# Kernel tuning notes

Hardware: AMD Instinct MI355X
Metric: run time of the kernel (lower is better)

## Reference

```python
import jax, jax.numpy as jnp
import numpy as np

C = 1.0          # Poincare ball curvature
EPS = 1e-7       # clamp epsilon used by the torch code


def _expmap0(u, c=C):
    # geoopt PoincareBall.expmap0: tanh(sqrt(c)||u||) * u / (sqrt(c)||u||)
    sc = jnp.sqrt(c)
    n = jnp.maximum(jnp.linalg.norm(u, axis=-1, keepdims=True), 1e-15)
    return jnp.tanh(sc * n) * u / (sc * n)


def _hyp_dist_sq(x, y, c=C):
    # Pairwise squared Poincare distance WITHOUT materializing [nq,nc,d]:
    # d(x,y) = (2/sqrt(c)) * artanh(sqrt(c) * ||mobius_add(-x, y)||)
    # ||mobius_add(-x,y)||^2 expands into dot products and squared norms.
    dot = x @ y.T                                  # [nq, nc]
    xn = jnp.sum(x * x, axis=-1)[:, None]          # [nq, 1]
    yn = jnp.sum(y * y, axis=-1)[None, :]          # [1, nc]
    alpha = 1.0 - 2.0 * c * dot + c * yn
    beta = 1.0 - c * xn
    num_sq = alpha * alpha * xn - 2.0 * alpha * beta * dot + beta * beta * yn
    den = jnp.maximum(1.0 - 2.0 * c * dot + c * c * xn * yn, 1e-15)
    t = jnp.sqrt(c) * jnp.sqrt(jnp.maximum(num_sq, 0.0)) / den
    t = jnp.clip(t, 0.0, 1.0 - EPS)
    d = (2.0 / jnp.sqrt(c)) * jnp.arctanh(t)
    return d * d


def _project(x, We, be, Wh, bh, Ws, bs, scale_h):
    e = x @ We.T + be
    e = e / jnp.linalg.norm(e, axis=-1, keepdims=True)
    h = _expmap0((x @ Wh.T + bh) * scale_h)
    s = x @ Ws.T + bs
    s = s / jnp.linalg.norm(s, axis=-1, keepdims=True)
    return e, h, s


def setup_inputs() -> dict:
    key = jax.random.key(0)
    ks = jax.random.split(key, 12)
    D, NQ, NC = 768, 512, 65536
    def lin(k, out_d, in_d):
        lim = 1.0 / np.sqrt(in_d)
        k1, k2 = jax.random.split(k)
        W = jax.random.uniform(k1, (out_d, in_d), jnp.float32, -lim, lim)
        b = jax.random.uniform(k2, (out_d,), jnp.float32, -lim, lim)
        return W, b
    We, be = lin(ks[0], 32, D)
    Wh, bh = lin(ks[1], 16, D)
    Ws, bs = lin(ks[2], 16, D)
    W1, b1 = lin(ks[3], 32, D)
    W2, b2 = lin(ks[4], 3, 32)
    return {
        'x_q': jax.random.normal(ks[5], (NQ, D), jnp.float32),
        'x_c': jax.random.normal(ks[6], (NC, D), jnp.float32),
        'We': We, 'be': be, 'Wh': Wh, 'bh': bh, 'Ws': Ws, 'bs': bs,
        'scale_h': jnp.float32(0.3),
        'W1': W1, 'b1': b1, 'W2': W2, 'b2': b2,
    }


def reference(x_q, x_c, We, be, Wh, bh, Ws, bs, scale_h, W1, b1, W2, b2):
    # forward() projections for queries and corpus
    q_e, q_h, q_s = _project(x_q, We, be, Wh, bh, Ws, bs, scale_h)
    c_e, c_h, c_s = _project(x_c, We, be, Wh, bh, Ws, bs, scale_h)
    # get_weights(): softplus MLP on raw query embedding -> [nq, 3]
    w = jax.nn.softplus(jax.nn.relu(x_q @ W1.T + b1) @ W2.T + b2)
    # batch_retrieve math, fully vectorized
    dist_e = 2.0 - 2.0 * (q_e @ c_e.T)                       # unit vecs: ||a-b||^2
    dots = jnp.clip(q_s @ c_s.T, -1.0 + EPS, 1.0 - EPS)
    dist_s = jnp.arccos(dots) ** 2
    dist_h = _hyp_dist_sq(q_h, c_h)
    total = w[:, 0:1] * dist_e + w[:, 1:2] * dist_h + w[:, 2:3] * dist_s
    return -total
```

## Files before the change

### kernel.cpp

```cpp
#include <hip/hip_runtime.h>
#include <math.h>

#define NQ 512
#define NC 65536
#define DIM 768
#define PC_ROWS 128

typedef unsigned short u16;
typedef float f32x4 __attribute__((ext_vector_type(4)));
typedef short bf16x8 __attribute__((ext_vector_type(8)));

#define MFMA16(A, B, C) __builtin_amdgcn_mfma_f32_16x16x32_bf16(A, B, C, 0, 0, 0)

__device__ __forceinline__ u16 f2bf(float x) {
  union { float f; unsigned int u; } v; v.f = x;
  unsigned int r = v.u + 0x7fffu + ((v.u >> 16) & 1u);
  return (u16)(r >> 16);
}
__device__ __forceinline__ float bf2f(u16 h) {
  union { unsigned int u; float f; } v; v.u = ((unsigned int)h) << 16;
  return v.f;
}
__device__ __forceinline__ unsigned int pk2(u16 a, u16 b) {
  return (unsigned int)a | ((unsigned int)b << 16);
}

__device__ __forceinline__ float acos_poly(float x) {
  float z = fabsf(x);
  float p = -0.0012624911f;
  p = fmaf(p, z, 0.0066700901f);
  p = fmaf(p, z, -0.0170881256f);
  p = fmaf(p, z, 0.0308918810f);
  p = fmaf(p, z, -0.0501743046f);
  p = fmaf(p, z, 0.0889789874f);
  p = fmaf(p, z, -0.2145988016f);
  p = fmaf(p, z, 1.5707963050f);
  float r = __builtin_amdgcn_sqrtf(1.0f - z) * p;
  return (x < 0.0f) ? (3.14159265358979f - r) : r;
}

__global__ __launch_bounds__(256) void build_wpak(
    const float* __restrict__ We, const float* __restrict__ Ws,
    const float* __restrict__ Wh, u16* __restrict__ wpak)
{
  int id = blockIdx.x * 256 + threadIdx.x;
  int j = id & 7;
  int lane = (id >> 3) & 63;
  int nt = (id >> 9) & 3;
  int kc = id >> 11;
  int o = nt * 16 + (lane & 15);
  int k = kc * 32 + ((lane >> 4) & 3) * 8 + j;
  const float* Wrow = (o < 32) ? We + (size_t)o * DIM
                    : (o < 48) ? Ws + (size_t)(o - 32) * DIM
                               : Wh + (size_t)(o - 48) * DIM;
  float w = Wrow[k];
  u16 hi = f2bf(w);
  u16 lo = f2bf(w - bf2f(hi));
  size_t base = (((size_t)kc * 4 + nt) * 2 * 64 + lane) * 8 + j;
  wpak[base] = hi;
  wpak[base + 512] = lo;
}

__global__ __launch_bounds__(128) void proj_q(
    const float* __restrict__ xq,
    const float* __restrict__ We, const float* __restrict__ be,
    const float* __restrict__ Wh, const float* __restrict__ bh,
    const float* __restrict__ Ws, const float* __restrict__ bs,
    const float* __restrict__ shp,
    const float* __restrict__ W1, const float* __restrict__ b1,
    const float* __restrict__ W2, const float* __restrict__ b2,
    u16* __restrict__ qpak, float* __restrict__ qmeta)
{
  __shared__ __align__(16) float xrow[DIM];
  __shared__ float vals[96];
  __shared__ float reluv[32];
  __shared__ float hv[16];
  __shared__ float stats[8];
  const int t = threadIdx.x;
  const int q = blockIdx.x;

  for (int i = t; i < DIM; i += 128) xrow[i] = xq[(size_t)q * DIM + i];
  __syncthreads();

  if (t < 96) {
    const float* wr;
    float bias;
    if (t < 32)      { wr = We + (size_t)t * DIM;        bias = be[t]; }
    else if (t < 48) { wr = Ws + (size_t)(t - 32) * DIM; bias = bs[t - 32]; }
    else if (t < 64) { wr = Wh + (size_t)(t - 48) * DIM; bias = bh[t - 48]; }
    else             { wr = W1 + (size_t)(t - 64) * DIM; bias = b1[t - 64]; }
    const float4* x4 = (const float4*)xrow;
    const float4* w4 = (const float4*)wr;
    float acc = 0.0f;
    #pragma unroll 4
    for (int k = 0; k < DIM / 4; ++k) {
      float4 a = x4[k];
      float4 b = w4[k];
      acc = fmaf(a.x, b.x, acc);
      acc = fmaf(a.y, b.y, acc);
      acc = fmaf(a.z, b.z, acc);
      acc = fmaf(a.w, b.w, acc);
    }
    acc += bias;
    if (t >= 48 && t < 64) acc *= shp[0];
    vals[t] = acc;
  }
  __syncthreads();
  if (t < 32) reluv[t] = fmaxf(vals[64 + t], 0.0f);
  __syncthreads();

  if (t == 0) {
    float s = 0.0f;
    for (int j = 0; j < 32; ++j) s += vals[j] * vals[j];
    stats[0] = sqrtf(s);
  } else if (t == 1) {
    float s = 0.0f;
    for (int j = 32; j < 48; ++j) s += vals[j] * vals[j];
    stats[1] = sqrtf(s);
  } else if (t == 2) {
    float s = 0.0f;
    for (int j = 48; j < 64; ++j) s += vals[j] * vals[j];
    float n = fmaxf(sqrtf(s), 1e-15f);
    float f = tanhf(n) / n;
    float xn = 0.0f;
    for (int j = 0; j < 16; ++j) {
      float hj = vals[48 + j] * f;
      hv[j] = hj;
      xn += hj * hj;
    }
    stats[2] = xn;
    stats[3] = 1.0f - xn;
  } else if (t >= 3 && t < 6) {
    int m = t - 3;
    float s = 0.0f;
    for (int j = 0; j < 32; ++j) s = fmaf(reluv[j], W2[m * 32 + j], s);
    s += b2[m];
    stats[4 + m] = fmaxf(s, 0.0f) + log1pf(expf(-fabsf(s)));
  }
  __syncthreads();

  u16* qp = qpak + (size_t)q * 192;
  if (t < 32) {
    float v = vals[t] / stats[0];
    u16 hi = f2bf(v);
    u16 lo = f2bf(v - bf2f(hi));
    qp[t] = hi; qp[32 + t] = lo;
  } else if (t < 48) {
    int j = t - 32;
    float v = vals[t] / stats[1];
    u16 hi = f2bf(v);
    u16 lo = f2bf(v - bf2f(hi));
    qp[64 + j] = hi;  qp[80 + j] = hi;
    qp[96 + j] = lo;  qp[112 + j] = lo;
  } else if (t < 64) {
    int j = t - 48;
    float v = hv[j];
    u16 hi = f2bf(v);
    u16 lo = f2bf(v - bf2f(hi));
    qp[128 + j] = hi; qp[144 + j] = hi;
    qp[160 + j] = lo; qp[176 + j] = lo;
  } else if (t == 64) qmeta[(size_t)q * 8 + 0] = stats[2];
  else if (t == 65)   qmeta[(size_t)q * 8 + 1] = stats[3];
  else if (t >= 66 && t < 69) qmeta[(size_t)q * 8 + (t - 66 + 2)] = stats[4 + (t - 66)];
}

__global__ __launch_bounds__(256) void proj_corpus(
    const float* __restrict__ xc, const u16* __restrict__ wpak,
    const float* __restrict__ be, const float* __restrict__ bh,
    const float* __restrict__ bs, const float* __restrict__ shp,
    u16* __restrict__ cpak, float* __restrict__ cyn)
{
  __shared__ float lds[8320];
  u16* xpk = (u16*)lds;
  float (*vals)[65] = (float(*)[65])lds;
  __shared__ float biasc[64];
  __shared__ float shv;

  const int tid = threadIdx.x;
  const int lane = tid & 63;
  const int wv = tid >> 6;
  const int lr = lane & 15;
  const int lg = lane >> 4;
  const int r0 = blockIdx.x * PC_ROWS;

  if (tid < 64) {
    biasc[tid] = (tid < 32) ? be[tid] : (tid < 48) ? bs[tid - 32] : bh[tid - 48];
    if (tid == 0) shv = shp[0];
  }

  f32x4 acc[2][4];
  #pragma unroll
  for (int rt = 0; rt < 2; ++rt)
    #pragma unroll
    for (int nt = 0; nt < 4; ++nt)
      acc[rt][nt] = (f32x4){0.0f, 0.0f, 0.0f, 0.0f};

  for (int kc = 0; kc < 24; ++kc) {
    __syncthreads();
    #pragma unroll
    for (int i = 0; i < 4; ++i) {
      int p = tid + 256 * i;
      int row = p >> 3;
      int kq = p & 7;
      const float4 v = *(const float4*)(xc + (size_t)(r0 + row) * DIM + kc * 32 + 4 * kq);
      u16 hx = f2bf(v.x), hy = f2bf(v.y), hz = f2bf(v.z), hw = f2bf(v.w);
      u16 lx = f2bf(v.x - bf2f(hx)), ly = f2bf(v.y - bf2f(hy));
      u16 lz = f2bf(v.z - bf2f(hz)), lw = f2bf(v.w - bf2f(hw));
      uint2 hvv = {pk2(hx, hy), pk2(hz, hw)};
      uint2 lvv = {pk2(lx, ly), pk2(lz, lw)};
      int rm = row & 7;
      int qh = (kq >> 1) ^ rm;
      int ql = (4 + (kq >> 1)) ^ rm;
      int half = (kq & 1) * 8;
      *(uint2*)((char*)xpk + row * 128 + qh * 16 + half) = hvv;
      *(uint2*)((char*)xpk + row * 128 + ql * 16 + half) = lvv;
    }
    __syncthreads();

    const u16* wb = wpak + (size_t)kc * 4096;
    bf16x8 Bh[4], Bl[4];
    #pragma unroll
    for (int nt = 0; nt < 4; ++nt) {
      Bh[nt] = *(const bf16x8*)(wb + (nt * 2 + 0) * 512 + lane * 8);
      Bl[nt] = *(const bf16x8*)(wb + (nt * 2 + 1) * 512 + lane * 8);
    }

    #pragma unroll
    for (int rt = 0; rt < 2; ++rt) {
      int rowi = wv * 32 + rt * 16 + lr;
      int rm = rowi & 7;
      bf16x8 Ah = *(const bf16x8*)((const char*)xpk + rowi * 128 + (lg ^ rm) * 16);
      bf16x8 Al = *(const bf16x8*)((const char*)xpk + rowi * 128 + ((4 + lg) ^ rm) * 16);
      #pragma unroll
      for (int nt = 0; nt < 4; ++nt) {
        acc[rt][nt] = MFMA16(Ah, Bh[nt], acc[rt][nt]);
        acc[rt][nt] = MFMA16(Al, Bh[nt], acc[rt][nt]);
        acc[rt][nt] = MFMA16(Ah, Bl[nt], acc[rt][nt]);
      }
    }
  }
  __syncthreads();

  #pragma unroll
  for (int rt = 0; rt < 2; ++rt)
    #pragma unroll
    for (int nt = 0; nt < 4; ++nt)
      #pragma unroll
      for (int reg = 0; reg < 4; ++reg) {
        int row = wv * 32 + rt * 16 + lg * 4 + reg;
        int o = nt * 16 + lr;
        float v = acc[rt][nt][reg] + biasc[o];
        if (o >= 48) v *= shv;
        vals[row][o] = v;
      }
  __syncthreads();

  const int part = tid >> 7;
  const int row = tid & 127;
  const size_t g = (size_t)(r0 + row);
  u16* cp = cpak + g * 128;
  if (part == 0) {
    float ssum = 0.0f;
    for (int j = 0; j < 32; ++j) ssum += vals[row][j] * vals[row][j];
    float inv = 1.0f / sqrtf(ssum);
    for (int j = 0; j < 32; ++j) {
      float v = vals[row][j] * inv;
      u16 hi = f2bf(v);
      cp[j] = hi;
      cp[32 + j] = f2bf(v - bf2f(hi));
    }
  } else {
    float ssum = 0.0f;
    for (int j = 32; j < 48; ++j) ssum += vals[row][j] * vals[row][j];
    float inv = 1.0f / sqrtf(ssum);
    for (int j = 0; j < 16; ++j) {
      float v = vals[row][32 + j] * inv;
      u16 hi = f2bf(v);
      cp[64 + j] = hi;
      cp[80 + j] = f2bf(v - bf2f(hi));
    }
    float hsum = 0.0f;
    for (int j = 48; j < 64; ++j) hsum += vals[row][j] * vals[row][j];
    float n = fmaxf(sqrtf(hsum), 1e-15f);
    float f = tanhf(n) / n;
    float yn = 0.0f;
    for (int j = 0; j < 16; ++j) {
      float hj = vals[row][48 + j] * f;
      u16 hi = f2bf(hj);
      cp[96 + j] = hi;
      cp[112 + j] = f2bf(hj - bf2f(hi));
      yn += hj * hj;
    }
    cyn[g] = yn;
  }
}

#define CLIPC 0.99999988f

__device__ __forceinline__ float pair_score(
    float de, float dss, float dh,
    float xn, float beta, float w0, float w1, float w2, float yn)
{
  float dist_e = 2.0f - 2.0f * de;

  float dcl = fminf(fmaxf(dss, -CLIPC), CLIPC);
  float ac = acos_poly(dcl);
  float dist_s = ac * ac;

  float alpha = 1.0f - 2.0f * dh + yn;
  float ab = alpha * beta;
  float num = alpha * alpha * xn - 2.0f * ab * dh + beta * beta * yn;
  float den = fmaxf(1.0f - 2.0f * dh + xn * yn, 1e-15f);
  float t = __builtin_amdgcn_sqrtf(fmaxf(num, 0.0f)) * __builtin_amdgcn_rcpf(den);
  t = fminf(t, CLIPC);
  float dd = __logf((1.0f + t) * __builtin_amdgcn_rcpf(1.0f - t));
  float dist_h = dd * dd;

  return -(w0 * dist_e + w1 * dist_h + w2 * dist_s);
}

__global__ __launch_bounds__(256) void pairwise(
    const u16* __restrict__ cpak, const float* __restrict__ cyn,
    const u16* __restrict__ qpak, const float* __restrict__ qmeta,
    float* __restrict__ out)
{
  const int lane = threadIdx.x & 63;
  const int wv = threadIdx.x >> 6;
  const int lr = lane & 15;
  const int lg = lane >> 4;
  const int c0 = blockIdx.x * 128 + wv * 32;
  const int qbase = blockIdx.y * 256;

  bf16x8 Beh[2], Bel[2], Bsp[2], Bhp[2];
  float ynv[2];
  #pragma unroll
  for (int ct = 0; ct < 2; ++ct) {
    const u16* cb = cpak + (size_t)(c0 + ct * 16 + lr) * 128 + lg * 8;
    Beh[ct] = *(const bf16x8*)(cb + 0);
    Bel[ct] = *(const bf16x8*)(cb + 32);
    Bsp[ct] = *(const bf16x8*)(cb + 64);
    Bhp[ct] = *(const bf16x8*)(cb + 96);
    ynv[ct] = cyn[c0 + ct * 16 + lr];
  }

  #pragma unroll 1
  for (int qt = 0; qt < 16; ++qt) {
    const int q0 = qbase + qt * 16;
    const u16* qb = qpak + (size_t)(q0 + lr) * 192 + lg * 8;
    bf16x8 Aeh = *(const bf16x8*)(qb + 0);
    bf16x8 Ael = *(const bf16x8*)(qb + 32);
    bf16x8 Ash = *(const bf16x8*)(qb + 64);
    bf16x8 Asl = *(const bf16x8*)(qb + 96);
    bf16x8 Ahh = *(const bf16x8*)(qb + 128);
    bf16x8 Ahl = *(const bf16x8*)(qb + 160);

    float4 mv[4];
    float w2v[4];
    #pragma unroll
    for (int j = 0; j < 4; ++j) {
      const int q = q0 + lg * 4 + j;
      mv[j] = *(const float4*)(qmeta + (size_t)q * 8);
      w2v[j] = qmeta[(size_t)q * 8 + 4];
    }

    const f32x4 z = {0.0f, 0.0f, 0.0f, 0.0f};
    f32x4 aE[2], aS[2], aH[2];
    #pragma unroll
    for (int ct = 0; ct < 2; ++ct) {
      aE[ct] = MFMA16(Aeh, Beh[ct], z);
      aE[ct] = MFMA16(Ael, Beh[ct], aE[ct]);
      aE[ct] = MFMA16(Aeh, Bel[ct], aE[ct]);
      aS[ct] = MFMA16(Ash, Bsp[ct], z);
      aS[ct] = MFMA16(Asl, Bsp[ct], aS[ct]);
      aH[ct] = MFMA16(Ahh, Bhp[ct], z);
      aH[ct] = MFMA16(Ahl, Bhp[ct], aH[ct]);
    }

    #pragma unroll
    for (int j = 0; j < 4; ++j) {
      const int q = q0 + lg * 4 + j;
      #pragma unroll
      for (int ct = 0; ct < 2; ++ct) {
        float r = pair_score(aE[ct][j], aS[ct][j], aH[ct][j],
                             mv[j].x, mv[j].y, mv[j].z, mv[j].w, w2v[j],
                             ynv[ct]);
        out[(size_t)q * NC + c0 + ct * 16 + lr] = r;
      }
    }
  }
}

extern "C" void kernel_launch(void* const* d_in, const int* in_sizes, int n_in,
                              void* d_out, int out_size, void* d_ws, size_t ws_size,
                              hipStream_t stream) {
  const float* xq = (const float*)d_in[0];
  const float* xc = (const float*)d_in[1];
  const float* We = (const float*)d_in[2];
  const float* be = (const float*)d_in[3];
  const float* Wh = (const float*)d_in[4];
  const float* bh = (const float*)d_in[5];
  const float* Ws = (const float*)d_in[6];
  const float* bs = (const float*)d_in[7];
  const float* sh = (const float*)d_in[8];
  const float* W1 = (const float*)d_in[9];
  const float* b1 = (const float*)d_in[10];
  const float* W2 = (const float*)d_in[11];
  const float* b2 = (const float*)d_in[12];
  float* out = (float*)d_out;

  float* w = (float*)d_ws;
  u16* qpak = (u16*)w;
  float* qmeta = w + 49152;
  u16* wpak = (u16*)(qmeta + NQ * 8);
  float* base2 = qmeta + NQ * 8 + 49152;
  u16* cpak = (u16*)base2;
  float* cyn = base2 + 4194304;

  build_wpak<<<192, 256, 0, stream>>>(We, Ws, Wh, wpak);
  proj_q<<<NQ, 128, 0, stream>>>(xq, We, be, Wh, bh, Ws, bs, sh, W1, b1, W2, b2,
                                 qpak, qmeta);
  proj_corpus<<<NC / PC_ROWS, 256, 0, stream>>>(xc, wpak, be, bh, bs, sh, cpak, cyn);
  pairwise<<<dim3(NC / 128, 2, 1), 256, 0, stream>>>(cpak, cyn, qpak, qmeta, out);
}
```

Measured before the change: 445.6 us.

## Pipeline corpus projection loads, precompute query metadata, simplify pairwise hyperbolic math

The corpus projection now stages raw fp32 rows into LDS with double-buffered direct global-to-LDS loads, one region per wave, and splits them into bf16 hi/lo pairs at fragment-load time with packed convert instructions. This removes the block-wide barriers and register conversion on the load path. The pairwise kernel caches per-query constants in LDS, prefetches the next query tile's operands, and rewrites the hyperbolic distance algebraically with a precomputed (1+yn) term so fewer ops run per pair. Output stores become nontemporal. The algebraic rewrite and the wider LDS footprint may change rounding and occupancy.

```diff
diff --git a/kernel.cpp b/kernel.cpp
--- a/kernel.cpp
+++ b/kernel.cpp
@@ -7,22 +7,30 @@
 #define PC_ROWS 128
 
 typedef unsigned short u16;
+typedef unsigned int u32;
 typedef float f32x4 __attribute__((ext_vector_type(4)));
 typedef short bf16x8 __attribute__((ext_vector_type(8)));
 
 #define MFMA16(A, B, C) __builtin_amdgcn_mfma_f32_16x16x32_bf16(A, B, C, 0, 0, 0)
 
 __device__ __forceinline__ u16 f2bf(float x) {
-  union { float f; unsigned int u; } v; v.f = x;
-  unsigned int r = v.u + 0x7fffu + ((v.u >> 16) & 1u);
+  union { float f; u32 u; } v; v.f = x;
+  u32 r = v.u + 0x7fffu + ((v.u >> 16) & 1u);
   return (u16)(r >> 16);
 }
 __device__ __forceinline__ float bf2f(u16 h) {
-  union { unsigned int u; float f; } v; v.u = ((unsigned int)h) << 16;
+  union { u32 u; float f; } v; v.u = ((u32)h) << 16;
   return v.f;
 }
-__device__ __forceinline__ unsigned int pk2(u16 a, u16 b) {
-  return (unsigned int)a | ((unsigned int)b << 16);
+__device__ __forceinline__ float u2f(u32 u) {
+  union { u32 u; float f; } v; v.u = u;
+  return v.f;
+}
+
+__device__ __forceinline__ u32 cvtpk(float a, float b) {
+  u32 r;
+  asm("v_cvt_pk_bf16_f32 %0, %1, %2" : "=v"(r) : "v"(a), "v"(b));
+  return r;
 }
 
 __device__ __forceinline__ float acos_poly(float x) {
@@ -159,9 +167,20 @@
     u16 lo = f2bf(v - bf2f(hi));
     qp[128 + j] = hi; qp[144 + j] = hi;
     qp[160 + j] = lo; qp[176 + j] = lo;
-  } else if (t == 64) qmeta[(size_t)q * 8 + 0] = stats[2];
-  else if (t == 65)   qmeta[(size_t)q * 8 + 1] = stats[3];
-  else if (t >= 66 && t < 69) qmeta[(size_t)q * 8 + (t - 66 + 2)] = stats[4 + (t - 66)];
+  } else if (t == 64) {
+    float xnv = stats[2];
+    float bet = stats[3];
+    float w0 = stats[4], w1v = stats[5], w2v = stats[6];
+    float* m = qmeta + (size_t)q * 8;
+    m[0] = xnv;
+    m[1] = bet * bet;
+    m[2] = -2.0f * (1.0f + xnv);
+    m[3] = -2.0f * w0;
+    m[4] = 2.0f * w0;
+    m[5] = w1v;
+    m[6] = w2v;
+    m[7] = 0.0f;
+  }
 }
 
 __global__ __launch_bounds__(256) void proj_corpus(
@@ -170,15 +189,14 @@
     const float* __restrict__ bs, const float* __restrict__ shp,
     u16* __restrict__ cpak, float* __restrict__ cyn)
 {
-  __shared__ float lds[8320];
-  u16* xpk = (u16*)lds;
-  float (*vals)[65] = (float(*)[65])lds;
+  __shared__ __align__(16) char smem[33280];
+  float (*vals)[65] = (float(*)[65])smem;
   __shared__ float biasc[64];
   __shared__ float shv;
 
   const int tid = threadIdx.x;
   const int lane = tid & 63;
-  const int wv = tid >> 6;
+  const int wv = __builtin_amdgcn_readfirstlane(tid >> 6);
   const int lr = lane & 15;
   const int lg = lane >> 4;
   const int r0 = blockIdx.x * PC_ROWS;
@@ -188,6 +206,22 @@
     if (tid == 0) shv = shp[0];
   }
 
+  const int row_w = lane >> 3;
+  const int qg = (lane & 7) ^ row_w;
+  const float* g0 = xc + (size_t)(r0 + wv * 32 +  0 + row_w) * DIM + qg * 4;
+  const float* g1 = xc + (size_t)(r0 + wv * 32 +  8 + row_w) * DIM + qg * 4;
+  const float* g2 = xc + (size_t)(r0 + wv * 32 + 16 + row_w) * DIM + qg * 4;
+  const float* g3 = xc + (size_t)(r0 + wv * 32 + 24 + row_w) * DIM + qg * 4;
+  char* sbase = smem + wv * 8192;
+
+#define STAGE(B, KC) do {                                                     \
+    char* d_ = sbase + (B) * 4096;                                            \
+    __builtin_amdgcn_global_load_lds(g0 + (KC) * 32, (void*)(d_       ), 16, 0, 0); \
+    __builtin_amdgcn_global_load_lds(g1 + (KC) * 32, (void*)(d_ + 1024), 16, 0, 0); \
+    __builtin_amdgcn_global_load_lds(g2 + (KC) * 32, (void*)(d_ + 2048), 16, 0, 0); \
+    __builtin_amdgcn_global_load_lds(g3 + (KC) * 32, (void*)(d_ + 3072), 16, 0, 0); \
+  } while (0)
+
   f32x4 acc[2][4];
   #pragma unroll
   for (int rt = 0; rt < 2; ++rt)
@@ -195,27 +229,11 @@
     for (int nt = 0; nt < 4; ++nt)
       acc[rt][nt] = (f32x4){0.0f, 0.0f, 0.0f, 0.0f};
 
+  STAGE(0, 0);
+
+  #pragma unroll 1
   for (int kc = 0; kc < 24; ++kc) {
-    __syncthreads();
-    #pragma unroll
-    for (int i = 0; i < 4; ++i) {
-      int p = tid + 256 * i;
-      int row = p >> 3;
-      int kq = p & 7;
-      const float4 v = *(const float4*)(xc + (size_t)(r0 + row) * DIM + kc * 32 + 4 * kq);
-      u16 hx = f2bf(v.x), hy = f2bf(v.y), hz = f2bf(v.z), hw = f2bf(v.w);
-      u16 lx = f2bf(v.x - bf2f(hx)), ly = f2bf(v.y - bf2f(hy));
-      u16 lz = f2bf(v.z - bf2f(hz)), lw = f2bf(v.w - bf2f(hw));
-      uint2 hvv = {pk2(hx, hy), pk2(hz, hw)};
-      uint2 lvv = {pk2(lx, ly), pk2(lz, lw)};
-      int rm = row & 7;
-      int qh = (kq >> 1) ^ rm;
-      int ql = (4 + (kq >> 1)) ^ rm;
-      int half = (kq & 1) * 8;
-      *(uint2*)((char*)xpk + row * 128 + qh * 16 + half) = hvv;
-      *(uint2*)((char*)xpk + row * 128 + ql * 16 + half) = lvv;
-    }
-    __syncthreads();
+    const int b = kc & 1;
 
     const u16* wb = wpak + (size_t)kc * 4096;
     bf16x8 Bh[4], Bl[4];
@@ -225,20 +243,44 @@
       Bl[nt] = *(const bf16x8*)(wb + (nt * 2 + 1) * 512 + lane * 8);
     }
 
+    if (kc < 23) {
+      STAGE(b ^ 1, kc + 1);
+      asm volatile("s_waitcnt vmcnt(4)" ::: "memory");
+    } else {
+      asm volatile("s_waitcnt vmcnt(0)" ::: "memory");
+    }
+
     #pragma unroll
     for (int rt = 0; rt < 2; ++rt) {
-      int rowi = wv * 32 + rt * 16 + lr;
-      int rm = rowi & 7;
-      bf16x8 Ah = *(const bf16x8*)((const char*)xpk + rowi * 128 + (lg ^ rm) * 16);
-      bf16x8 Al = *(const bf16x8*)((const char*)xpk + rowi * 128 + ((4 + lg) ^ rm) * 16);
+      const int rwl = rt * 16 + lr;
+      const int rm = rwl & 7;
+      const char* rb = sbase + b * 4096 + rwl * 128;
+      const int q0s = (2 * lg) ^ rm;
+      f32x4 a0 = *(const f32x4*)(rb + q0s * 16);
+      f32x4 a1 = *(const f32x4*)(rb + (q0s ^ 1) * 16);
+
+      u32 h0 = cvtpk(a0.x, a0.y);
+      u32 h1 = cvtpk(a0.z, a0.w);
+      u32 h2 = cvtpk(a1.x, a1.y);
+      u32 h3 = cvtpk(a1.z, a1.w);
+      u32 l0 = cvtpk(a0.x - u2f(h0 << 16), a0.y - u2f(h0 & 0xffff0000u));
+      u32 l1 = cvtpk(a0.z - u2f(h1 << 16), a0.w - u2f(h1 & 0xffff0000u));
+      u32 l2 = cvtpk(a1.x - u2f(h2 << 16), a1.y - u2f(h2 & 0xffff0000u));
+      u32 l3 = cvtpk(a1.z - u2f(h3 << 16), a1.w - u2f(h3 & 0xffff0000u));
+      union { u32 u[4]; bf16x8 v; } Ah, Al;
+      Ah.u[0] = h0; Ah.u[1] = h1; Ah.u[2] = h2; Ah.u[3] = h3;
+      Al.u[0] = l0; Al.u[1] = l1; Al.u[2] = l2; Al.u[3] = l3;
+
       #pragma unroll
       for (int nt = 0; nt < 4; ++nt) {
-        acc[rt][nt] = MFMA16(Ah, Bh[nt], acc[rt][nt]);
-        acc[rt][nt] = MFMA16(Al, Bh[nt], acc[rt][nt]);
-        acc[rt][nt] = MFMA16(Ah, Bl[nt], acc[rt][nt]);
+        acc[rt][nt] = MFMA16(Ah.v, Bh[nt], acc[rt][nt]);
+        acc[rt][nt] = MFMA16(Al.v, Bh[nt], acc[rt][nt]);
+        acc[rt][nt] = MFMA16(Ah.v, Bl[nt], acc[rt][nt]);
       }
     }
   }
+#undef STAGE
+
   __syncthreads();
 
   #pragma unroll
@@ -298,25 +340,26 @@
 #define CLIPC 0.99999988f
 
 __device__ __forceinline__ float pair_score(
-    float de, float dss, float dh,
-    float xn, float beta, float w0, float w1, float w2, float yn)
+    float de, float dss, float u,
+    float4 mA, float4 mB, float yn, float yp1, float yp2)
 {
-  float dist_e = 2.0f - 2.0f * de;
+  float eterm = fmaf(de, mA.w, mB.x);
 
   float dcl = fminf(fmaxf(dss, -CLIPC), CLIPC);
   float ac = acos_poly(dcl);
-  float dist_s = ac * ac;
-
-  float alpha = 1.0f - 2.0f * dh + yn;
-  float ab = alpha * beta;
-  float num = alpha * alpha * xn - 2.0f * ab * dh + beta * beta * yn;
-  float den = fmaxf(1.0f - 2.0f * dh + xn * yn, 1e-15f);
-  float t = __builtin_amdgcn_sqrtf(fmaxf(num, 0.0f)) * __builtin_amdgcn_rcpf(den);
-  t = fminf(t, CLIPC);
-  float dd = __logf((1.0f + t) * __builtin_amdgcn_rcpf(1.0f - t));
-  float dist_h = dd * dd;
-
-  return -(w0 * dist_e + w1 * dist_h + w2 * dist_s);
+  float sterm = mB.z * ac * ac;
+
+  float Pm  = mA.z * yp1;
+  float t1  = fmaf(4.0f, u, Pm);
+  float C   = fmaf(mA.x, yp2, mA.y * yn);
+  float num = fmaf(u, t1, C);
+  float den = fmaf(-2.0f, u, fmaf(mA.x, yn, 1.0f));
+  float s = __builtin_amdgcn_sqrtf(fmaxf(num, 0.0f));
+  s = fminf(s, CLIPC * den);
+  float dd = __logf((den + s) * __builtin_amdgcn_rcpf(den - s));
+  float hterm = mB.y * dd * dd;
+
+  return -(eterm + hterm + sterm);
 }
 
 __global__ __launch_bounds__(256) void pairwise(
@@ -324,15 +367,24 @@
     const u16* __restrict__ qpak, const float* __restrict__ qmeta,
     float* __restrict__ out)
 {
-  const int lane = threadIdx.x & 63;
-  const int wv = threadIdx.x >> 6;
+  __shared__ float4 lmA[NQ];
+  __shared__ float4 lmB[NQ];
+  const int tid = threadIdx.x;
+  for (int i = tid; i < NQ; i += 256) {
+    const float4* m = (const float4*)(qmeta + (size_t)i * 8);
+    lmA[i] = m[0];
+    lmB[i] = m[1];
+  }
+
+  const int lane = tid & 63;
+  const int wv = tid >> 6;
   const int lr = lane & 15;
   const int lg = lane >> 4;
   const int c0 = blockIdx.x * 128 + wv * 32;
   const int qbase = blockIdx.y * 256;
 
   bf16x8 Beh[2], Bel[2], Bsp[2], Bhp[2];
-  float ynv[2];
+  float ynv[2], yp1v[2], yp2v[2];
   #pragma unroll
   for (int ct = 0; ct < 2; ++ct) {
     const u16* cb = cpak + (size_t)(c0 + ct * 16 + lr) * 128 + lg * 8;
@@ -340,28 +392,33 @@
     Bel[ct] = *(const bf16x8*)(cb + 32);
     Bsp[ct] = *(const bf16x8*)(cb + 64);
     Bhp[ct] = *(const bf16x8*)(cb + 96);
-    ynv[ct] = cyn[c0 + ct * 16 + lr];
-  }
-
-  #pragma unroll 1
+    float yn = cyn[c0 + ct * 16 + lr];
+    ynv[ct] = yn;
+    yp1v[ct] = 1.0f + yn;
+    yp2v[ct] = yp1v[ct] * yp1v[ct];
+  }
+  __syncthreads();
+
+  const u16* qb = qpak + (size_t)(qbase + lr) * 192 + lg * 8;
+  bf16x8 Aeh = *(const bf16x8*)(qb + 0);
+  bf16x8 Ael = *(const bf16x8*)(qb + 32);
+  bf16x8 Ash = *(const bf16x8*)(qb + 64);
+  bf16x8 Asl = *(const bf16x8*)(qb + 96);
+  bf16x8 Ahh = *(const bf16x8*)(qb + 128);
+  bf16x8 Ahl = *(const bf16x8*)(qb + 160);
+
+  #pragma unroll 2
   for (int qt = 0; qt < 16; ++qt) {
     const int q0 = qbase + qt * 16;
-    const u16* qb = qpak + (size_t)(q0 + lr) * 192 + lg * 8;
-    bf16x8 Aeh = *(const bf16x8*)(qb + 0);
-    bf16x8 Ael = *(const bf16x8*)(qb + 32);
-    bf16x8 Ash = *(const bf16x8*)(qb + 64);
-    bf16x8 Asl = *(const bf16x8*)(qb + 96);
-    bf16x8 Ahh = *(const bf16x8*)(qb + 128);
-    bf16x8 Ahl = *(const bf16x8*)(qb + 160);
-
-    float4 mv[4];
-    float w2v[4];
-    #pragma unroll
-    for (int j = 0; j < 4; ++j) {
-      const int q = q0 + lg * 4 + j;
-      mv[j] = *(const float4*)(qmeta + (size_t)q * 8);
-      w2v[j] = qmeta[(size_t)q * 8 + 4];
-    }
+
+    const int qtn = (qt < 15) ? qt + 1 : qt;
+    const u16* qn = qpak + (size_t)(qbase + qtn * 16 + lr) * 192 + lg * 8;
+    bf16x8 Neh = *(const bf16x8*)(qn + 0);
+    bf16x8 Nel = *(const bf16x8*)(qn + 32);
+    bf16x8 Nsh = *(const bf16x8*)(qn + 64);
+    bf16x8 Nsl = *(const bf16x8*)(qn + 96);
+    bf16x8 Nhh = *(const bf16x8*)(qn + 128);
+    bf16x8 Nhl = *(const bf16x8*)(qn + 160);
 
     const f32x4 z = {0.0f, 0.0f, 0.0f, 0.0f};
     f32x4 aE[2], aS[2], aH[2];
@@ -379,14 +436,17 @@
     #pragma unroll
     for (int j = 0; j < 4; ++j) {
       const int q = q0 + lg * 4 + j;
+      const float4 mA = lmA[q];
+      const float4 mB = lmB[q];
       #pragma unroll
       for (int ct = 0; ct < 2; ++ct) {
         float r = pair_score(aE[ct][j], aS[ct][j], aH[ct][j],
-                             mv[j].x, mv[j].y, mv[j].z, mv[j].w, w2v[j],
-                             ynv[ct]);
-        out[(size_t)q * NC + c0 + ct * 16 + lr] = r;
+                             mA, mB, ynv[ct], yp1v[ct], yp2v[ct]);
+        __builtin_nontemporal_store(r, &out[(size_t)q * NC + c0 + ct * 16 + lr]);
       }
     }
+
+    Aeh = Neh; Ael = Nel; Ash = Nsh; Asl = Nsl; Ahh = Nhh; Ahl = Nhl;
   }
 }
 
```

Result: faster. 424.7 us (-4.7%).
